# Kernel optimization log

Measured on AMD Instinct MI355X. Metric: run time of the kernel, lower is better.

The kernel has to match this reference:

```python
import jax, jax.numpy as jnp
import numpy as np

DIM = 128
N = 2048
M = 2048


def setup_inputs() -> dict:
    key = jax.random.key(0)
    k1, k2, k3, k4, k5, k6 = jax.random.split(key, 6)
    s1 = 1.0 / np.sqrt(2 * DIM)  # torch Linear default init bound
    s2 = 1.0 / np.sqrt(DIM)
    return {
        "z_i": jax.random.normal(k1, (N, DIM), dtype=jnp.float32),
        "z_j": jax.random.normal(k2, (M, DIM), dtype=jnp.float32),
        "W1": jax.random.uniform(k3, (2 * DIM, DIM), minval=-s1, maxval=s1, dtype=jnp.float32),
        "b1": jax.random.uniform(k4, (DIM,), minval=-s1, maxval=s1, dtype=jnp.float32),
        "W2": jax.random.uniform(k5, (DIM, 1), minval=-s2, maxval=s2, dtype=jnp.float32),
        "b2": jax.random.uniform(k6, (1,), minval=-s2, maxval=s2, dtype=jnp.float32),
    }


def reference(z_i, z_j, W1, b1, W2, b2):
    # Linear(cat([zi, zj])) == zi @ W1[:dim] + zj @ W1[dim:] + b1 -- same math
    # as the torch module, without materializing the [N, M, 2*dim] concat.
    hi = z_i @ W1[:DIM]  # [N, dim]
    hj = z_j @ W1[DIM:]  # [M, dim]
    h = jax.nn.relu(hi[:, None, :] + hj[None, :, :] + b1)  # [N, M, dim]
    out = h @ W2 + b2  # [N, M, 1]
    return out[..., 0]  # [N, M]
```

## Files before the change

kernel.cpp:

```cpp
#include <hip/hip_runtime.h>

#define DIM 128
#define NROWS 2048

typedef float v2f __attribute__((ext_vector_type(2)));

__global__ __launch_bounds__(256) void prep_kernel(
    const float* __restrict__ z_i, const float* __restrict__ z_j,
    const float* __restrict__ W1, const float* __restrict__ b1,
    float* __restrict__ hiT, float* __restrict__ hjbT) {
  __shared__ float zsT[DIM * 65];
  __shared__ float wt[DIM * 16];

  const int t = threadIdx.x;
  const int side = blockIdx.z;
  const int rowbase = blockIdx.x * 64;
  const int d0 = blockIdx.y * 16;
  const float* z = side ? z_j : z_i;
  const float* w = W1 + side * (DIM * DIM);

#pragma unroll
  for (int jj = 0; jj < 8; ++jj) {
    const int idx = t + jj * 256;
    const int row = idx >> 5;
    const int kc = (idx & 31) * 4;
    const float4 v = *(const float4*)(z + (size_t)(rowbase + row) * DIM + kc);
    zsT[(kc + 0) * 65 + row] = v.x;
    zsT[(kc + 1) * 65 + row] = v.y;
    zsT[(kc + 2) * 65 + row] = v.z;
    zsT[(kc + 3) * 65 + row] = v.w;
  }
#pragma unroll
  for (int jj = 0; jj < 2; ++jj) {
    const int idx = t + jj * 256;
    const int k = idx >> 2;
    const int c = (idx & 3) * 4;
    *(float4*)(wt + k * 16 + c) = *(const float4*)(w + k * DIM + d0 + c);
  }
  __syncthreads();

  const int r = t & 63;
  const int dg = t >> 6;
  v2f acc0 = {0.f, 0.f}, acc1 = {0.f, 0.f};

#pragma unroll 8
  for (int k = 0; k < DIM; ++k) {
    const float zv = zsT[k * 65 + r];
    const float4 wv = *(const float4*)(wt + k * 16 + dg * 4);
    const v2f zv2 = {zv, zv};
    acc0 = __builtin_elementwise_fma((v2f){wv.x, wv.y}, zv2, acc0);
    acc1 = __builtin_elementwise_fma((v2f){wv.z, wv.w}, zv2, acc1);
  }

  float* dst = (side ? hjbT : hiT);
  const int dglobal = d0 + dg * 4;
  float bias[4] = {0.f, 0.f, 0.f, 0.f};
  if (side) {
#pragma unroll
    for (int q = 0; q < 4; ++q) bias[q] = b1[dglobal + q];
  }
  const float res[4] = {acc0.x, acc0.y, acc1.x, acc1.y};
#pragma unroll
  for (int q = 0; q < 4; ++q)
    dst[(size_t)(dglobal + q) * NROWS + rowbase + r] = res[q] + bias[q];
}

__global__ __launch_bounds__(256) void score_kernel(
    const float* __restrict__ hiT, const float* __restrict__ hjbT,
    const float* __restrict__ W2, const float* __restrict__ b2p,
    float* __restrict__ out) {
  __shared__ float his[32 * 64];
  __shared__ float hjs[32 * 64];

  const int t = threadIdx.x;
  const int tx = t & 15;
  const int ty = t >> 4;
  const int ibase = blockIdx.y * 64;
  const int jbase = blockIdx.x * 64;

  const int srow = t >> 4;
  const int scol = (t & 15) * 4;

  v2f acc[4][2];
#pragma unroll
  for (int ii = 0; ii < 4; ++ii)
#pragma unroll
    for (int jj = 0; jj < 2; ++jj) acc[ii][jj] = (v2f){0.f, 0.f};

  float4 bufA[2], bufB[2];
#pragma unroll
  for (int k = 0; k < 2; ++k) {
    const int row = srow + 16 * k;
    bufA[k] = *(const float4*)(hiT + (size_t)row * NROWS + ibase + scol);
    bufB[k] = *(const float4*)(hjbT + (size_t)row * NROWS + jbase + scol);
  }

  for (int c = 0; c < 4; ++c) {
    const int d0 = c * 32;
#pragma unroll
    for (int k = 0; k < 2; ++k) {
      *(float4*)(his + (srow + 16 * k) * 64 + scol) = bufA[k];
      *(float4*)(hjs + (srow + 16 * k) * 64 + scol) = bufB[k];
    }
    __syncthreads();

    if (c < 3) {
      const int dn = d0 + 32;
#pragma unroll
      for (int k = 0; k < 2; ++k) {
        const int row = dn + srow + 16 * k;
        bufA[k] = *(const float4*)(hiT + (size_t)row * NROWS + ibase + scol);
        bufB[k] = *(const float4*)(hjbT + (size_t)row * NROWS + jbase + scol);
      }
    }

#pragma unroll 4
    for (int d = 0; d < 32; ++d) {
      const float wv = W2[d0 + d];
      const float4 hv = *(const float4*)(his + d * 64 + ty * 4);
      const float4 jv = *(const float4*)(hjs + d * 64 + tx * 4);
      const float hi4[4] = {hv.x, hv.y, hv.z, hv.w};
      const v2f hjv[2] = {{jv.x, jv.y}, {jv.z, jv.w}};
      const v2f wv2 = {wv, wv};
      const v2f zero = {0.f, 0.f};
#pragma unroll
      for (int ii = 0; ii < 4; ++ii) {
        const v2f hb = {hi4[ii], hi4[ii]};
#pragma unroll
        for (int jj = 0; jj < 2; ++jj) {
          v2f s = hb + hjv[jj];
          s = __builtin_elementwise_max(s, zero);
          acc[ii][jj] = __builtin_elementwise_fma(s, wv2, acc[ii][jj]);
        }
      }
    }
    __syncthreads();
  }

  const float bias = *b2p;
#pragma unroll
  for (int ii = 0; ii < 4; ++ii) {
    const int i = ibase + ty * 4 + ii;
    float* o = out + (size_t)i * NROWS + jbase + tx * 4;
    const float4 ov = {acc[ii][0].x + bias, acc[ii][0].y + bias,
                       acc[ii][1].x + bias, acc[ii][1].y + bias};
    *(float4*)o = ov;
  }
}

extern "C" void kernel_launch(void* const* d_in, const int* in_sizes, int n_in,
                              void* d_out, int out_size, void* d_ws, size_t ws_size,
                              hipStream_t stream) {
  const float* z_i = (const float*)d_in[0];
  const float* z_j = (const float*)d_in[1];
  const float* W1  = (const float*)d_in[2];
  const float* b1  = (const float*)d_in[3];
  const float* W2  = (const float*)d_in[4];
  const float* b2  = (const float*)d_in[5];
  float* out = (float*)d_out;

  float* hiT  = (float*)d_ws;
  float* hjbT = hiT + (size_t)DIM * NROWS;

  prep_kernel<<<dim3(32, 8, 2), 256, 0, stream>>>(z_i, z_j, W1, b1, hiT, hjbT);
  score_kernel<<<dim3(32, 32), 256, 0, stream>>>(hiT, hjbT, W2, b2, out);
}
```

Measured before the change: 116.0 us.

## Use packed fp16 math with fdot2 for pairwise score and larger tiles

Stores the projected hi/hj vectors as packed half2 pairs. The score kernel does its add and relu in packed fp16 and accumulates with v_dot2 (fdot2) into fp32, which halves the inner-loop instruction count per pair. The score tile grows to 64x128 with all 128 dims loaded to LDS up front, and the prep kernel is restructured to hold all of W1 in LDS. Reduced precision in the add/relu could cost accuracy against the fp32 reference.

```diff
diff --git a/kernel.cpp b/kernel.cpp
--- a/kernel.cpp
+++ b/kernel.cpp
@@ -2,149 +2,126 @@
 
 #define DIM 128
 #define NROWS 2048
+#define NDP 64
 
 typedef float v2f __attribute__((ext_vector_type(2)));
+typedef _Float16 h2 __attribute__((ext_vector_type(2)));
 
-__global__ __launch_bounds__(256) void prep_kernel(
+static __device__ __forceinline__ h2 u2h(unsigned u) { return __builtin_bit_cast(h2, u); }
+static __device__ __forceinline__ unsigned h2u(h2 h) { return __builtin_bit_cast(unsigned, h); }
+
+__global__ __launch_bounds__(512) void prep_kernel(
     const float* __restrict__ z_i, const float* __restrict__ z_j,
     const float* __restrict__ W1, const float* __restrict__ b1,
-    float* __restrict__ hiT, float* __restrict__ hjbT) {
-  __shared__ float zsT[DIM * 65];
-  __shared__ float wt[DIM * 16];
+    unsigned* __restrict__ hi2T, unsigned* __restrict__ hj2T) {
+  __shared__ float wlds[DIM * DIM];
 
   const int t = threadIdx.x;
-  const int side = blockIdx.z;
-  const int rowbase = blockIdx.x * 64;
-  const int d0 = blockIdx.y * 16;
-  const float* z = side ? z_j : z_i;
+  const int side = blockIdx.y;
+  const int rowbase = blockIdx.x * 8;
   const float* w = W1 + side * (DIM * DIM);
 
 #pragma unroll
-  for (int jj = 0; jj < 8; ++jj) {
-    const int idx = t + jj * 256;
-    const int row = idx >> 5;
-    const int kc = (idx & 31) * 4;
-    const float4 v = *(const float4*)(z + (size_t)(rowbase + row) * DIM + kc);
-    zsT[(kc + 0) * 65 + row] = v.x;
-    zsT[(kc + 1) * 65 + row] = v.y;
-    zsT[(kc + 2) * 65 + row] = v.z;
-    zsT[(kc + 3) * 65 + row] = v.w;
-  }
-#pragma unroll
-  for (int jj = 0; jj < 2; ++jj) {
-    const int idx = t + jj * 256;
-    const int k = idx >> 2;
-    const int c = (idx & 3) * 4;
-    *(float4*)(wt + k * 16 + c) = *(const float4*)(w + k * DIM + d0 + c);
+  for (int rep = 0; rep < 8; ++rep) {
+    const int idx = rep * 512 + t;
+    *(float4*)(wlds + idx * 4) = *(const float4*)(w + idx * 4);
   }
   __syncthreads();
 
-  const int r = t & 63;
-  const int dg = t >> 6;
-  v2f acc0 = {0.f, 0.f}, acc1 = {0.f, 0.f};
+  const int row = rowbase + (t >> 6);
+  const int dp = t & 63;
+  const float* zrow = (side ? z_j : z_i) + (size_t)row * DIM;
 
+  v2f acc = {0.f, 0.f};
 #pragma unroll 8
   for (int k = 0; k < DIM; ++k) {
-    const float zv = zsT[k * 65 + r];
-    const float4 wv = *(const float4*)(wt + k * 16 + dg * 4);
-    const v2f zv2 = {zv, zv};
-    acc0 = __builtin_elementwise_fma((v2f){wv.x, wv.y}, zv2, acc0);
-    acc1 = __builtin_elementwise_fma((v2f){wv.z, wv.w}, zv2, acc1);
+    const float zv = zrow[k];
+    const v2f wv = *(const v2f*)(wlds + k * DIM + dp * 2);
+    acc = __builtin_elementwise_fma(wv, (v2f){zv, zv}, acc);
   }
 
-  float* dst = (side ? hjbT : hiT);
-  const int dglobal = d0 + dg * 4;
-  float bias[4] = {0.f, 0.f, 0.f, 0.f};
   if (side) {
-#pragma unroll
-    for (int q = 0; q < 4; ++q) bias[q] = b1[dglobal + q];
+    acc.x += b1[2 * dp];
+    acc.y += b1[2 * dp + 1];
   }
-  const float res[4] = {acc0.x, acc0.y, acc1.x, acc1.y};
-#pragma unroll
-  for (int q = 0; q < 4; ++q)
-    dst[(size_t)(dglobal + q) * NROWS + rowbase + r] = res[q] + bias[q];
+  h2 hv = {(_Float16)acc.x, (_Float16)acc.y};
+  unsigned* dst = side ? hj2T : hi2T;
+  dst[(size_t)dp * NROWS + row] = h2u(hv);
 }
 
 __global__ __launch_bounds__(256) void score_kernel(
-    const float* __restrict__ hiT, const float* __restrict__ hjbT,
+    const unsigned* __restrict__ hi2T, const unsigned* __restrict__ hj2T,
     const float* __restrict__ W2, const float* __restrict__ b2p,
     float* __restrict__ out) {
-  __shared__ float his[32 * 64];
-  __shared__ float hjs[32 * 64];
+  __shared__ unsigned his2[NDP * 64];
+  __shared__ unsigned hjs2[NDP * 128];
+  __shared__ unsigned w2s[NDP];
 
   const int t = threadIdx.x;
+  const int ibase = blockIdx.y * 64;
+  const int jbase = blockIdx.x * 128;
+
+#pragma unroll
+  for (int rep = 0; rep < 4; ++rep) {
+    const int idx = rep * 256 + t;
+    const int dp = idx >> 4, c = (idx & 15) * 4;
+    *(uint4*)(his2 + dp * 64 + c) =
+        *(const uint4*)(hi2T + (size_t)dp * NROWS + ibase + c);
+  }
+#pragma unroll
+  for (int rep = 0; rep < 8; ++rep) {
+    const int idx = rep * 256 + t;
+    const int dp = idx >> 5, c = (idx & 31) * 4;
+    *(uint4*)(hjs2 + dp * 128 + c) =
+        *(const uint4*)(hj2T + (size_t)dp * NROWS + jbase + c);
+  }
+  if (t < NDP) {
+    h2 wp = {(_Float16)W2[2 * t], (_Float16)W2[2 * t + 1]};
+    w2s[t] = h2u(wp);
+  }
+  __syncthreads();
+
   const int tx = t & 15;
   const int ty = t >> 4;
-  const int ibase = blockIdx.y * 64;
-  const int jbase = blockIdx.x * 64;
 
-  const int srow = t >> 4;
-  const int scol = (t & 15) * 4;
-
-  v2f acc[4][2];
+  float acc[4][8];
 #pragma unroll
   for (int ii = 0; ii < 4; ++ii)
 #pragma unroll
-    for (int jj = 0; jj < 2; ++jj) acc[ii][jj] = (v2f){0.f, 0.f};
+    for (int jj = 0; jj < 8; ++jj) acc[ii][jj] = 0.f;
 
-  float4 bufA[2], bufB[2];
+#pragma unroll 8
+  for (int dp = 0; dp < NDP; ++dp) {
+    const uint4 hu = *(const uint4*)(his2 + dp * 64 + ty * 4);
+    const uint4 ju0 = *(const uint4*)(hjs2 + dp * 128 + tx * 8);
+    const uint4 ju1 = *(const uint4*)(hjs2 + dp * 128 + tx * 8 + 4);
+    const h2 wp = u2h(w2s[dp]);
+    const h2 hiv[4] = {u2h(hu.x), u2h(hu.y), u2h(hu.z), u2h(hu.w)};
+    const h2 hjv[8] = {u2h(ju0.x), u2h(ju0.y), u2h(ju0.z), u2h(ju0.w),
+                       u2h(ju1.x), u2h(ju1.y), u2h(ju1.z), u2h(ju1.w)};
+    const h2 zero = {(_Float16)0.f, (_Float16)0.f};
 #pragma unroll
-  for (int k = 0; k < 2; ++k) {
-    const int row = srow + 16 * k;
-    bufA[k] = *(const float4*)(hiT + (size_t)row * NROWS + ibase + scol);
-    bufB[k] = *(const float4*)(hjbT + (size_t)row * NROWS + jbase + scol);
-  }
-
-  for (int c = 0; c < 4; ++c) {
-    const int d0 = c * 32;
+    for (int ii = 0; ii < 4; ++ii) {
 #pragma unroll
-    for (int k = 0; k < 2; ++k) {
-      *(float4*)(his + (srow + 16 * k) * 64 + scol) = bufA[k];
-      *(float4*)(hjs + (srow + 16 * k) * 64 + scol) = bufB[k];
-    }
-    __syncthreads();
-
-    if (c < 3) {
-      const int dn = d0 + 32;
-#pragma unroll
-      for (int k = 0; k < 2; ++k) {
-        const int row = dn + srow + 16 * k;
-        bufA[k] = *(const float4*)(hiT + (size_t)row * NROWS + ibase + scol);
-        bufB[k] = *(const float4*)(hjbT + (size_t)row * NROWS + jbase + scol);
+      for (int jj = 0; jj < 8; ++jj) {
+        h2 s = hiv[ii] + hjv[jj];
+        s = __builtin_elementwise_max(s, zero);
+        acc[ii][jj] = __builtin_amdgcn_fdot2(s, wp, acc[ii][jj], false);
       }
     }
-
-#pragma unroll 4
-    for (int d = 0; d < 32; ++d) {
-      const float wv = W2[d0 + d];
-      const float4 hv = *(const float4*)(his + d * 64 + ty * 4);
-      const float4 jv = *(const float4*)(hjs + d * 64 + tx * 4);
-      const float hi4[4] = {hv.x, hv.y, hv.z, hv.w};
-      const v2f hjv[2] = {{jv.x, jv.y}, {jv.z, jv.w}};
-      const v2f wv2 = {wv, wv};
-      const v2f zero = {0.f, 0.f};
-#pragma unroll
-      for (int ii = 0; ii < 4; ++ii) {
-        const v2f hb = {hi4[ii], hi4[ii]};
-#pragma unroll
-        for (int jj = 0; jj < 2; ++jj) {
-          v2f s = hb + hjv[jj];
-          s = __builtin_elementwise_max(s, zero);
-          acc[ii][jj] = __builtin_elementwise_fma(s, wv2, acc[ii][jj]);
-        }
-      }
-    }
-    __syncthreads();
   }
 
   const float bias = *b2p;
 #pragma unroll
   for (int ii = 0; ii < 4; ++ii) {
     const int i = ibase + ty * 4 + ii;
-    float* o = out + (size_t)i * NROWS + jbase + tx * 4;
-    const float4 ov = {acc[ii][0].x + bias, acc[ii][0].y + bias,
-                       acc[ii][1].x + bias, acc[ii][1].y + bias};
-    *(float4*)o = ov;
+    float* o = out + (size_t)i * NROWS + jbase + tx * 8;
+    const float4 o0 = {acc[ii][0] + bias, acc[ii][1] + bias,
+                       acc[ii][2] + bias, acc[ii][3] + bias};
+    const float4 o1 = {acc[ii][4] + bias, acc[ii][5] + bias,
+                       acc[ii][6] + bias, acc[ii][7] + bias};
+    *(float4*)o = o0;
+    *(float4*)(o + 4) = o1;
   }
 }
 
@@ -159,9 +136,9 @@
   const float* b2  = (const float*)d_in[5];
   float* out = (float*)d_out;
 
-  float* hiT  = (float*)d_ws;
-  float* hjbT = hiT + (size_t)DIM * NROWS;
+  unsigned* hi2T = (unsigned*)d_ws;
+  unsigned* hj2T = hi2T + (size_t)NDP * NROWS;
 
-  prep_kernel<<<dim3(32, 8, 2), 256, 0, stream>>>(z_i, z_j, W1, b1, hiT, hjbT);
-  score_kernel<<<dim3(32, 32), 256, 0, stream>>>(hiT, hjbT, W2, b2, out);
+  prep_kernel<<<dim3(256, 2), 512, 0, stream>>>(z_i, z_j, W1, b1, hi2T, hj2T);
+  score_kernel<<<dim3(16, 32), 256, 0, stream>>>(hi2T, hj2T, W2, b2, out);
 }
```

Result: faster. 106.2 us (-8.4%).
